# Kernel optimization log

Hardware: AMD Instinct MI355X
Metric: run time of the kernel (lower is better)

## Reference

```python
import jax, jax.numpy as jnp
import numpy as np

HEADS = 4
DIM_HEAD = 32
SCALE = 10.0
EPS = 1e-12

def l2norm_axis1(t):
    # Faithful to source: default axis=1 -> normalize over the SEQUENCE axis of [B,N,h,d]
    denom = jnp.clip(jnp.linalg.norm(t, ord=2, axis=1, keepdims=True), EPS)
    return t / denom

def setup_inputs() -> dict:
    key = jax.random.key(0)
    k1, k2, k3 = jax.random.split(key, 3)
    B, N, C = 4, 4096, 128
    dim = HEADS * DIM_HEAD  # 128
    x = jax.random.normal(k1, (B, N, C), dtype=jnp.float32)
    W_qkv = jax.random.normal(k2, (C, 3 * dim), dtype=jnp.float32) * (1.0 / np.sqrt(C))
    W_out = jax.random.normal(k3, (dim, C), dtype=jnp.float32) * (1.0 / np.sqrt(dim))
    b_out = jnp.zeros((C,), dtype=jnp.float32)
    return {"x": x, "W_qkv": W_qkv, "W_out": W_out, "b_out": b_out}

def reference(x, W_qkv, W_out, b_out):
    B, N, C = x.shape
    # 1x1 conv == per-token linear
    qkv = jnp.einsum('bnc,ce->bne', x, W_qkv)  # [B,N,3*dim]
    q, k, v = jnp.split(qkv, 3, axis=-1)
    # [B,N,h,d]
    q = q.reshape(B, N, HEADS, DIM_HEAD)
    k = k.reshape(B, N, HEADS, DIM_HEAD)
    v = v.reshape(B, N, HEADS, DIM_HEAD)
    q = l2norm_axis1(q)
    k = l2norm_axis1(k)
    sim = jnp.einsum('bihd,bjhd->bhij', q, k) * SCALE  # [B,h,N,N]
    attn = jax.nn.softmax(sim, axis=-1)
    out = jnp.einsum('bhij,bjhd->bhid', attn, v)  # [B,h,N,d]
    out = out.transpose(0, 2, 1, 3).reshape(B, N, HEADS * DIM_HEAD)  # [B,N,dim]
    return jnp.einsum('bne,ec->bnc', out, W_out) + b_out
```

## Files before the change

kernel.cpp:

```cpp
#include <hip/hip_runtime.h>

typedef short s16x8 __attribute__((ext_vector_type(8)));
typedef short s16x4 __attribute__((ext_vector_type(4)));
typedef float f32x4 __attribute__((ext_vector_type(4)));
typedef float f4 __attribute__((ext_vector_type(4)));
typedef unsigned short u16x4 __attribute__((ext_vector_type(4)));

#define CEXP 14.426950408889634074f

__device__ __forceinline__ unsigned short f2bf(float f) {
    union { float f; unsigned int i; } v; v.f = f;
    unsigned int x = v.i;
    return (unsigned short)((x + 0x7fffu + ((x >> 16) & 1u)) >> 16);
}
__device__ __forceinline__ float bf2f(unsigned short u) {
    union { unsigned int i; float f; } v; v.i = ((unsigned int)u) << 16; return v.f;
}

__device__ __forceinline__ f32x4 mfma16x16x16_bf16(s16x4 a, s16x4 b, f32x4 c) {
#if __has_builtin(__builtin_amdgcn_mfma_f32_16x16x16bf16_1k)
    return __builtin_amdgcn_mfma_f32_16x16x16bf16_1k(a, b, c, 0, 0, 0);
#else
    f32x4 d = c;
    asm("v_mfma_f32_16x16x16_bf16 %0, %1, %2, %0" : "+v"(d) : "v"(a), "v"(b));
    return d;
#endif
}

__global__ __launch_bounds__(256) void k_prep(
    const float* __restrict__ x, const float* __restrict__ Wqkv,
    const float* __restrict__ Wout,
    unsigned short* __restrict__ xb, unsigned short* __restrict__ Wt,
    unsigned short* __restrict__ WoT)
{
    const int blk = blockIdx.x, tid = threadIdx.x;
    if (blk < 1024) {
        int base = (blk * 256 + tid) * 8;
        f4 a = *(const f4*)&x[base];
        f4 b = *(const f4*)&x[base + 4];
        u16x4 p0 = { f2bf(a[0]), f2bf(a[1]), f2bf(a[2]), f2bf(a[3]) };
        u16x4 p1 = { f2bf(b[0]), f2bf(b[1]), f2bf(b[2]), f2bf(b[3]) };
        *(u16x4*)&xb[base] = p0;
        *(u16x4*)&xb[base + 4] = p1;
    } else if (blk < 1216) {
        int e = (blk - 1024) * 256 + tid;
        int n = e >> 7, k = e & 127;
        Wt[e] = f2bf(Wqkv[k * 384 + n]);
    } else {
        int e = (blk - 1216) * 256 + tid;
        int n = e >> 7, k = e & 127;
        WoT[e] = f2bf(Wout[k * 128 + n]);
    }
}

__global__ __launch_bounds__(256, 4) void k_qkv(
    const unsigned short* __restrict__ xb, const unsigned short* __restrict__ Wt,
    unsigned short* __restrict__ Qb, unsigned short* __restrict__ Kb,
    unsigned short* __restrict__ Vt, float* __restrict__ sumsq)
{
    const int tid = threadIdx.x;
    const int wl = tid >> 6, lane = tid & 63;
    const int qd = lane >> 4, nn = lane & 15;
    const int n0 = blockIdx.y * 64;
    const int tw0 = blockIdx.x * 64 + wl * 16;

    f32x4 acc[4];
#pragma unroll
    for (int nb = 0; nb < 4; ++nb) acc[nb] = (f32x4){0.f, 0.f, 0.f, 0.f};

    const unsigned short* ap = xb + (size_t)(tw0 + nn) * 128 + qd * 8;
    const unsigned short* bp = Wt + (size_t)(n0 + nn) * 128 + qd * 8;
#pragma unroll
    for (int ks = 0; ks < 4; ++ks) {
        s16x8 af = *(const s16x8*)(ap + ks * 32);
#pragma unroll
        for (int nb = 0; nb < 4; ++nb) {
            s16x8 bf = *(const s16x8*)(bp + (size_t)nb * 16 * 128 + ks * 32);
            acc[nb] = __builtin_amdgcn_mfma_f32_16x16x32_bf16(af, bf, acc[nb], 0, 0, 0);
        }
    }

    const int cb = n0 >> 7;
    const int cbase = n0 & 127;
    const int b = tw0 >> 12;
    const int tl0 = tw0 & 4095;

    if (cb < 2) {
        unsigned short* dst = (cb == 0) ? Qb : Kb;
#pragma unroll
        for (int nb = 0; nb < 4; ++nb) {
            const int dim = cbase + nb * 16 + nn;
            const int h = dim >> 5, d = dim & 31;
            unsigned short* base = dst + (size_t)((b * 4 + h) * 4096 + tl0 + qd * 4) * 32 + d;
#pragma unroll
            for (int r = 0; r < 4; ++r)
                base[r * 32] = f2bf(acc[nb][r]);
            float ss = acc[nb][0]*acc[nb][0] + acc[nb][1]*acc[nb][1]
                     + acc[nb][2]*acc[nb][2] + acc[nb][3]*acc[nb][3];
            ss += __shfl_xor(ss, 16);
            ss += __shfl_xor(ss, 32);
            if (qd == 0)
                atomicAdd(&sumsq[cb * 512 + (b * 4 + h) * 32 + d], ss);
        }
    } else {
#pragma unroll
        for (int nb = 0; nb < 4; ++nb) {
            const int dim = cbase + nb * 16 + nn;
            const int h = dim >> 5, d = dim & 31;
            u16x4 pk = { f2bf(acc[nb][0]), f2bf(acc[nb][1]),
                         f2bf(acc[nb][2]), f2bf(acc[nb][3]) };
            *(u16x4*)&Vt[(size_t)((b * 4 + h) * 32 + d) * 4096 + tl0 + qd * 4] = pk;
        }
    }
}

__global__ __launch_bounds__(256) void k_norm(
    unsigned short* __restrict__ Qb, unsigned short* __restrict__ Kb,
    const float* __restrict__ sumsq)
{
    int t = blockIdx.x * 256 + threadIdx.x;
    int which = t >> 18;
    int ti = t & 0x3ffff;
    unsigned short* arr = which ? Kb : Qb;
    const float post = which ? 1.0f : CEXP;
    int i8 = ti * 8;
    int d0 = i8 & 31;
    int bh = i8 >> 17;
    const float* sq = sumsq + which * 512 + bh * 32 + d0;
    union { uint4 v; unsigned short u[8]; } dat;
    dat.v = *(const uint4*)(arr + i8);
#pragma unroll
    for (int j = 0; j < 8; ++j) {
        float r = fminf(__builtin_amdgcn_rsqf(sq[j]), 1e12f) * post;
        dat.u[j] = f2bf(bf2f(dat.u[j]) * r);
    }
    *(uint4*)(arr + i8) = dat.v;
}

__global__ __launch_bounds__(512, 4) void k_attn(
    const unsigned short* __restrict__ Qb, const unsigned short* __restrict__ Kb,
    const unsigned short* __restrict__ Vt, unsigned short* __restrict__ Ogb)
{
    __shared__ char smem[32768];
    const int tid  = threadIdx.x;
    const int wv   = tid >> 6, lane = tid & 63;
    const int wl   = wv & 3, half = wv >> 2;
    const int qd   = lane >> 4, nn = lane & 15;
    const int bh   = blockIdx.x;
    const int ib   = blockIdx.y * 64 + wl * 16;
    const unsigned short* Qbh = Qb + (size_t)bh * 4096 * 32;
    const unsigned short* Kbh = Kb + (size_t)bh * 4096 * 32;
    const unsigned short* Vbh = Vt + (size_t)bh * 32 * 4096;

    s16x8 qfrag = *(const s16x8*)(Qbh + (ib + nn) * 32 + qd * 8);
    f32x4 o0 = {0.f,0.f,0.f,0.f}, o1 = {0.f,0.f,0.f,0.f};
    const f32x4 zro = {0.f,0.f,0.f,0.f};
    float lp = 0.f;

    const int KB0 = half * 8192;
    const int VB0 = 16384 + half * 8192;
    const int jb0 = half * 2048;

    const unsigned short* ksrc = Kbh + (size_t)(jb0 + wl * 16 + nn) * 32 + qd * 8;
    const unsigned short* vsrc = Vbh + (size_t)(nn + 16 * (wl >> 1)) * 4096
                               + jb0 + ((wl & 1) * 2 + (qd >> 1)) * 16 + (qd & 1) * 8;
    char* kdst = smem + KB0 + wl * 1024 + lane * 16;
    char* vdst = smem + VB0 + wl * 1024 + lane * 16;

    {
        uint4 gk = *(const uint4*)ksrc;
        uint4 gv = *(const uint4*)vsrc;
        ksrc += 2048; vsrc += 64;
        *(uint4*)kdst = gk;
        *(uint4*)vdst = gv;
    }

    const int vro = (qd >> 1) * 256 + nn * 16 + (qd & 1) * 8;

    for (int jt = 0; jt < 32; ++jt) {
        uint4 ngk = *(const uint4*)ksrc;
        uint4 ngv = *(const uint4*)vsrc;
        ksrc += 2048; vsrc += 64;

        __syncthreads();
        const char* kcur = smem + KB0 + (jt & 1) * 4096;
        const char* vcur = smem + VB0 + (jt & 1) * 4096;
#pragma unroll
        for (int js = 0; js < 4; ++js) {
            s16x8 kf = *(const s16x8*)(kcur + js * 1024 + lane * 16);
            f32x4 sv = __builtin_amdgcn_mfma_f32_16x16x32_bf16(kf, qfrag, zro, 0, 0, 0);
            float p0 = __builtin_amdgcn_exp2f(sv[0]);
            float p1 = __builtin_amdgcn_exp2f(sv[1]);
            float p2 = __builtin_amdgcn_exp2f(sv[2]);
            float p3 = __builtin_amdgcn_exp2f(sv[3]);
            lp += (p0 + p1) + (p2 + p3);
            unsigned u0 = __float_as_uint(p0) + 0x8000u;
            unsigned u1 = __float_as_uint(p1) + 0x8000u;
            unsigned u2 = __float_as_uint(p2) + 0x8000u;
            unsigned u3 = __float_as_uint(p3) + 0x8000u;
            union { uint2 u; s16x4 s; } pb;
            pb.u.x = __builtin_amdgcn_perm(u1, u0, 0x07060302u);
            pb.u.y = __builtin_amdgcn_perm(u3, u2, 0x07060302u);
            s16x4 va = *(const s16x4*)(vcur + js * 512 + vro);
            s16x4 vb = *(const s16x4*)(vcur + 2048 + js * 512 + vro);
            o0 = mfma16x16x16_bf16(va, pb.s, o0);
            o1 = mfma16x16x16_bf16(vb, pb.s, o1);
        }
        const int nxt4k = ((jt + 1) & 1) * 4096;
        *(uint4*)(kdst + nxt4k) = ngk;
        *(uint4*)(vdst + nxt4k) = ngv;
    }

    lp += __shfl_xor(lp, 16);
    lp += __shfl_xor(lp, 32);
    __syncthreads();
    float* Ob = (float*)smem;
    float* Lb = (float*)(smem + 8192);
    if (half) {
        float* d = Ob + (wl * 64 + lane) * 8;
        *(f4*)d = o0; *(f4*)(d + 4) = o1;
        Lb[wl * 64 + lane] = lp;
    }
    __syncthreads();
    if (!half) {
        float* d = Ob + (wl * 64 + lane) * 8;
        f4 a0 = *(const f4*)d, a1 = *(const f4*)(d + 4);
        float rl = 1.f / (lp + Lb[wl * 64 + lane]);
        o0 = (o0 + a0) * rl;
        o1 = (o1 + a1) * rl;
        u16x4 pk0 = { f2bf(o0[0]), f2bf(o0[1]), f2bf(o0[2]), f2bf(o0[3]) };
        u16x4 pk1 = { f2bf(o1[0]), f2bf(o1[1]), f2bf(o1[2]), f2bf(o1[3]) };
        const int bb = bh >> 2, hh = bh & 3;
        unsigned short* dst = Ogb + (size_t)(bb * 4096 + blockIdx.y * 64 + wl * 16 + nn) * 128
                            + hh * 32 + qd * 4;
        *(u16x4*)dst = pk0;
        *(u16x4*)(dst + 16) = pk1;
    }
}

__global__ __launch_bounds__(256, 4) void k_out(
    const unsigned short* __restrict__ Ogb, const unsigned short* __restrict__ WoT,
    const float* __restrict__ bout, float* __restrict__ out)
{
    const int tid = threadIdx.x;
    const int wl = tid >> 6, lane = tid & 63;
    const int qd = lane >> 4, nn = lane & 15;
    const int n0 = blockIdx.y * 64;
    const int tw0 = blockIdx.x * 64 + wl * 16;

    f32x4 acc[4];
#pragma unroll
    for (int nb = 0; nb < 4; ++nb) acc[nb] = (f32x4){0.f, 0.f, 0.f, 0.f};

    const unsigned short* ap = WoT + (size_t)(n0 + nn) * 128 + qd * 8;
    const unsigned short* bp = Ogb + (size_t)(tw0 + nn) * 128 + qd * 8;
#pragma unroll
    for (int ks = 0; ks < 4; ++ks) {
        s16x8 bf = *(const s16x8*)(bp + ks * 32);
#pragma unroll
        for (int nb = 0; nb < 4; ++nb) {
            s16x8 af = *(const s16x8*)(ap + (size_t)nb * 16 * 128 + ks * 32);
            acc[nb] = __builtin_amdgcn_mfma_f32_16x16x32_bf16(af, bf, acc[nb], 0, 0, 0);
        }
    }
#pragma unroll
    for (int nb = 0; nb < 4; ++nb) {
        const int c = n0 + nb * 16 + qd * 4;
        f4 bv = *(const f4*)&bout[c];
        f4 r;
#pragma unroll
        for (int j = 0; j < 4; ++j) r[j] = acc[nb][j] + bv[j];
        *(f4*)&out[(size_t)(tw0 + nn) * 128 + c] = r;
    }
}

extern "C" void kernel_launch(void* const* d_in, const int* in_sizes, int n_in,
                              void* d_out, int out_size, void* d_ws, size_t ws_size,
                              hipStream_t stream)
{
    const float* x    = (const float*)d_in[0];
    const float* Wqkv = (const float*)d_in[1];
    const float* Wout = (const float*)d_in[2];
    const float* bout = (const float*)d_in[3];
    float* out = (float*)d_out;
    char* ws = (char*)d_ws;
    const size_t MB = 1024 * 1024;
    unsigned short* Qb  = (unsigned short*)(ws);
    unsigned short* Kb  = (unsigned short*)(ws + 4 * MB);
    unsigned short* Vt  = (unsigned short*)(ws + 8 * MB);
    unsigned short* Ogb = (unsigned short*)(ws + 12 * MB);
    unsigned short* xb  = (unsigned short*)(ws + 16 * MB);
    unsigned short* Wt  = (unsigned short*)(ws + 20 * MB);
    unsigned short* WoT = (unsigned short*)(ws + 20 * MB + 112 * 1024);
    float*        sumsq = (float*)(ws + 20 * MB + 160 * 1024);

    hipMemsetAsync(sumsq, 0, 4096, stream);
    hipLaunchKernelGGL(k_prep, dim3(1280), dim3(256), 0, stream, x, Wqkv, Wout, xb, Wt, WoT);
    hipLaunchKernelGGL(k_qkv, dim3(256, 6), dim3(256), 0, stream, xb, Wt, Qb, Kb, Vt, sumsq);
    hipLaunchKernelGGL(k_norm, dim3(2048), dim3(256), 0, stream, Qb, Kb, sumsq);
    hipLaunchKernelGGL(k_attn, dim3(16, 64), dim3(512), 0, stream, Qb, Kb, Vt, Ogb);
    hipLaunchKernelGGL(k_out, dim3(256, 2), dim3(256), 0, stream, Ogb, WoT, bout, out);
}
```

Before: 169.1 us.

## Process two query tiles per wave in attention and fold Q normalization in

After: 189.8 us. 12.2% more time.

```diff
diff --git a/kernel.cpp b/kernel.cpp
--- a/kernel.cpp
+++ b/kernel.cpp
@@ -27,6 +27,30 @@
 #endif
 }
 
+__device__ __forceinline__ s16x4 pk_bf16x4(float p0, float p1, float p2, float p3) {
+#if __has_builtin(__builtin_amdgcn_cvt_pk_bf16_f32)
+    typedef __bf16 bf16x2 __attribute__((ext_vector_type(2)));
+    union { struct { bf16x2 a, b; } h; s16x4 s; } r;
+    r.h.a = __builtin_amdgcn_cvt_pk_bf16_f32(p0, p1);
+    r.h.b = __builtin_amdgcn_cvt_pk_bf16_f32(p2, p3);
+    return r.s;
+#else
+    unsigned u0 = __float_as_uint(p0) + 0x8000u;
+    unsigned u1 = __float_as_uint(p1) + 0x8000u;
+    unsigned u2 = __float_as_uint(p2) + 0x8000u;
+    unsigned u3 = __float_as_uint(p3) + 0x8000u;
+    union { uint2 u; s16x4 s; } pb;
+    pb.u.x = __builtin_amdgcn_perm(u1, u0, 0x07060302u);
+    pb.u.y = __builtin_amdgcn_perm(u3, u2, 0x07060302u);
+    return pb.s;
+#endif
+}
+
+__device__ __forceinline__ u16x4 pk4(f4 v) {
+    u16x4 r = { f2bf(v[0]), f2bf(v[1]), f2bf(v[2]), f2bf(v[3]) };
+    return r;
+}
+
 __global__ __launch_bounds__(256) void k_prep(
     const float* __restrict__ x, const float* __restrict__ Wqkv,
     const float* __restrict__ Wout,
@@ -38,10 +62,8 @@
         int base = (blk * 256 + tid) * 8;
         f4 a = *(const f4*)&x[base];
         f4 b = *(const f4*)&x[base + 4];
-        u16x4 p0 = { f2bf(a[0]), f2bf(a[1]), f2bf(a[2]), f2bf(a[3]) };
-        u16x4 p1 = { f2bf(b[0]), f2bf(b[1]), f2bf(b[2]), f2bf(b[3]) };
-        *(u16x4*)&xb[base] = p0;
-        *(u16x4*)&xb[base + 4] = p1;
+        *(u16x4*)&xb[base] = pk4(a);
+        *(u16x4*)&xb[base + 4] = pk4(b);
     } else if (blk < 1216) {
         int e = (blk - 1024) * 256 + tid;
         int n = e >> 7, k = e & 127;
@@ -64,82 +86,91 @@
     const int n0 = blockIdx.y * 64;
     const int tw0 = blockIdx.x * 64 + wl * 16;
 
-    f32x4 acc[4];
-#pragma unroll
-    for (int nb = 0; nb < 4; ++nb) acc[nb] = (f32x4){0.f, 0.f, 0.f, 0.f};
-
     const unsigned short* ap = xb + (size_t)(tw0 + nn) * 128 + qd * 8;
     const unsigned short* bp = Wt + (size_t)(n0 + nn) * 128 + qd * 8;
-#pragma unroll
-    for (int ks = 0; ks < 4; ++ks) {
-        s16x8 af = *(const s16x8*)(ap + ks * 32);
-#pragma unroll
-        for (int nb = 0; nb < 4; ++nb) {
-            s16x8 bf = *(const s16x8*)(bp + (size_t)nb * 16 * 128 + ks * 32);
-            acc[nb] = __builtin_amdgcn_mfma_f32_16x16x32_bf16(af, bf, acc[nb], 0, 0, 0);
-        }
-    }
+    s16x8 af[4], bfr[16];
+#pragma unroll
+    for (int ks = 0; ks < 4; ++ks) af[ks] = *(const s16x8*)(ap + ks * 32);
+#pragma unroll
+    for (int nb = 0; nb < 4; ++nb)
+#pragma unroll
+        for (int ks = 0; ks < 4; ++ks)
+            bfr[nb * 4 + ks] = *(const s16x8*)(bp + (size_t)nb * 2048 + ks * 32);
+
+    f32x4 acc[4];
+#pragma unroll
+    for (int nb = 0; nb < 4; ++nb) acc[nb] = (f32x4){0.f, 0.f, 0.f, 0.f};
 
     const int cb = n0 >> 7;
-    const int cbase = n0 & 127;
     const int b = tw0 >> 12;
     const int tl0 = tw0 & 4095;
 
     if (cb < 2) {
+#pragma unroll
+        for (int ks = 0; ks < 4; ++ks)
+#pragma unroll
+            for (int nb = 0; nb < 4; ++nb)
+                acc[nb] = __builtin_amdgcn_mfma_f32_16x16x32_bf16(bfr[nb * 4 + ks], af[ks], acc[nb], 0, 0, 0);
         unsigned short* dst = (cb == 0) ? Qb : Kb;
+        const int tok = tl0 + nn;
 #pragma unroll
         for (int nb = 0; nb < 4; ++nb) {
-            const int dim = cbase + nb * 16 + nn;
-            const int h = dim >> 5, d = dim & 31;
-            unsigned short* base = dst + (size_t)((b * 4 + h) * 4096 + tl0 + qd * 4) * 32 + d;
-#pragma unroll
-            for (int r = 0; r < 4; ++r)
-                base[r * 32] = f2bf(acc[nb][r]);
-            float ss = acc[nb][0]*acc[nb][0] + acc[nb][1]*acc[nb][1]
-                     + acc[nb][2]*acc[nb][2] + acc[nb][3]*acc[nb][3];
-            ss += __shfl_xor(ss, 16);
-            ss += __shfl_xor(ss, 32);
-            if (qd == 0)
-                atomicAdd(&sumsq[cb * 512 + (b * 4 + h) * 32 + d], ss);
+            const int dim = (n0 & 127) + nb * 16 + qd * 4;
+            const int h = dim >> 5, d0 = dim & 31;
+            *(u16x4*)&dst[(size_t)((b * 4 + h) * 4096 + tok) * 32 + d0] = pk4(acc[nb]);
+            f32x4 ss;
+#pragma unroll
+            for (int r = 0; r < 4; ++r) ss[r] = acc[nb][r] * acc[nb][r];
+#pragma unroll
+            for (int m = 1; m < 16; m <<= 1) {
+#pragma unroll
+                for (int r = 0; r < 4; ++r) ss[r] += __shfl_xor(ss[r], m);
+            }
+            if (nn == 0) {
+                float* sp = &sumsq[cb * 512 + (b * 4 + h) * 32 + d0];
+                atomicAdd(sp + 0, ss[0]);
+                atomicAdd(sp + 1, ss[1]);
+                atomicAdd(sp + 2, ss[2]);
+                atomicAdd(sp + 3, ss[3]);
+            }
         }
     } else {
 #pragma unroll
+        for (int ks = 0; ks < 4; ++ks)
+#pragma unroll
+            for (int nb = 0; nb < 4; ++nb)
+                acc[nb] = __builtin_amdgcn_mfma_f32_16x16x32_bf16(af[ks], bfr[nb * 4 + ks], acc[nb], 0, 0, 0);
+#pragma unroll
         for (int nb = 0; nb < 4; ++nb) {
-            const int dim = cbase + nb * 16 + nn;
+            const int dim = (n0 & 127) + nb * 16 + nn;
             const int h = dim >> 5, d = dim & 31;
-            u16x4 pk = { f2bf(acc[nb][0]), f2bf(acc[nb][1]),
-                         f2bf(acc[nb][2]), f2bf(acc[nb][3]) };
-            *(u16x4*)&Vt[(size_t)((b * 4 + h) * 32 + d) * 4096 + tl0 + qd * 4] = pk;
+            *(u16x4*)&Vt[(size_t)((b * 4 + h) * 32 + d) * 4096 + tl0 + qd * 4] = pk4(acc[nb]);
         }
     }
 }
 
 __global__ __launch_bounds__(256) void k_norm(
-    unsigned short* __restrict__ Qb, unsigned short* __restrict__ Kb,
-    const float* __restrict__ sumsq)
+    unsigned short* __restrict__ Kb, const float* __restrict__ sumsq)
 {
     int t = blockIdx.x * 256 + threadIdx.x;
-    int which = t >> 18;
-    int ti = t & 0x3ffff;
-    unsigned short* arr = which ? Kb : Qb;
-    const float post = which ? 1.0f : CEXP;
-    int i8 = ti * 8;
+    int i8 = t * 8;
     int d0 = i8 & 31;
     int bh = i8 >> 17;
-    const float* sq = sumsq + which * 512 + bh * 32 + d0;
+    const float* sq = sumsq + 512 + bh * 32 + d0;
     union { uint4 v; unsigned short u[8]; } dat;
-    dat.v = *(const uint4*)(arr + i8);
+    dat.v = *(const uint4*)(Kb + i8);
 #pragma unroll
     for (int j = 0; j < 8; ++j) {
-        float r = fminf(__builtin_amdgcn_rsqf(sq[j]), 1e12f) * post;
+        float r = fminf(__builtin_amdgcn_rsqf(sq[j]), 1e12f);
         dat.u[j] = f2bf(bf2f(dat.u[j]) * r);
     }
-    *(uint4*)(arr + i8) = dat.v;
-}
-
-__global__ __launch_bounds__(512, 4) void k_attn(
+    *(uint4*)(Kb + i8) = dat.v;
+}
+
+__global__ __launch_bounds__(512, 2) void k_attn(
     const unsigned short* __restrict__ Qb, const unsigned short* __restrict__ Kb,
-    const unsigned short* __restrict__ Vt, unsigned short* __restrict__ Ogb)
+    const unsigned short* __restrict__ Vt, const float* __restrict__ sumsq,
+    unsigned short* __restrict__ Ogb)
 {
     __shared__ char smem[32768];
     const int tid  = threadIdx.x;
@@ -147,15 +178,30 @@
     const int wl   = wv & 3, half = wv >> 2;
     const int qd   = lane >> 4, nn = lane & 15;
     const int bh   = blockIdx.x;
-    const int ib   = blockIdx.y * 64 + wl * 16;
+    const int ib   = blockIdx.y * 128 + wl * 32;
     const unsigned short* Qbh = Qb + (size_t)bh * 4096 * 32;
     const unsigned short* Kbh = Kb + (size_t)bh * 4096 * 32;
     const unsigned short* Vbh = Vt + (size_t)bh * 32 * 4096;
 
-    s16x8 qfrag = *(const s16x8*)(Qbh + (ib + nn) * 32 + qd * 8);
-    f32x4 o0 = {0.f,0.f,0.f,0.f}, o1 = {0.f,0.f,0.f,0.f};
+    float rj[8];
+    const float* sqq = sumsq + bh * 32 + qd * 8;
+#pragma unroll
+    for (int j = 0; j < 8; ++j)
+        rj[j] = fminf(__builtin_amdgcn_rsqf(sqq[j]), 1e12f) * CEXP;
+
+    s16x8 q0r = *(const s16x8*)(Qbh + (ib + nn) * 32 + qd * 8);
+    s16x8 q1r = *(const s16x8*)(Qbh + (ib + 16 + nn) * 32 + qd * 8);
+    s16x8 qf0, qf1;
+#pragma unroll
+    for (int j = 0; j < 8; ++j) {
+        qf0[j] = (short)f2bf(bf2f((unsigned short)q0r[j]) * rj[j]);
+        qf1[j] = (short)f2bf(bf2f((unsigned short)q1r[j]) * rj[j]);
+    }
+
+    f32x4 o00 = {0.f,0.f,0.f,0.f}, o01 = {0.f,0.f,0.f,0.f};
+    f32x4 o10 = {0.f,0.f,0.f,0.f}, o11 = {0.f,0.f,0.f,0.f};
     const f32x4 zro = {0.f,0.f,0.f,0.f};
-    float lp = 0.f;
+    float lpa = 0.f, lpb = 0.f;
 
     const int KB0 = half * 8192;
     const int VB0 = 16384 + half * 8192;
@@ -188,53 +234,65 @@
 #pragma unroll
         for (int js = 0; js < 4; ++js) {
             s16x8 kf = *(const s16x8*)(kcur + js * 1024 + lane * 16);
-            f32x4 sv = __builtin_amdgcn_mfma_f32_16x16x32_bf16(kf, qfrag, zro, 0, 0, 0);
-            float p0 = __builtin_amdgcn_exp2f(sv[0]);
-            float p1 = __builtin_amdgcn_exp2f(sv[1]);
-            float p2 = __builtin_amdgcn_exp2f(sv[2]);
-            float p3 = __builtin_amdgcn_exp2f(sv[3]);
-            lp += (p0 + p1) + (p2 + p3);
-            unsigned u0 = __float_as_uint(p0) + 0x8000u;
-            unsigned u1 = __float_as_uint(p1) + 0x8000u;
-            unsigned u2 = __float_as_uint(p2) + 0x8000u;
-            unsigned u3 = __float_as_uint(p3) + 0x8000u;
-            union { uint2 u; s16x4 s; } pb;
-            pb.u.x = __builtin_amdgcn_perm(u1, u0, 0x07060302u);
-            pb.u.y = __builtin_amdgcn_perm(u3, u2, 0x07060302u);
+            f32x4 sa = __builtin_amdgcn_mfma_f32_16x16x32_bf16(kf, qf0, zro, 0, 0, 0);
+            f32x4 sb = __builtin_amdgcn_mfma_f32_16x16x32_bf16(kf, qf1, zro, 0, 0, 0);
+            float a0 = __builtin_amdgcn_exp2f(sa[0]);
+            float a1 = __builtin_amdgcn_exp2f(sa[1]);
+            float a2 = __builtin_amdgcn_exp2f(sa[2]);
+            float a3 = __builtin_amdgcn_exp2f(sa[3]);
+            float b0 = __builtin_amdgcn_exp2f(sb[0]);
+            float b1 = __builtin_amdgcn_exp2f(sb[1]);
+            float b2 = __builtin_amdgcn_exp2f(sb[2]);
+            float b3 = __builtin_amdgcn_exp2f(sb[3]);
+            lpa += (a0 + a1) + (a2 + a3);
+            lpb += (b0 + b1) + (b2 + b3);
+            s16x4 pa = pk_bf16x4(a0, a1, a2, a3);
+            s16x4 pb = pk_bf16x4(b0, b1, b2, b3);
             s16x4 va = *(const s16x4*)(vcur + js * 512 + vro);
             s16x4 vb = *(const s16x4*)(vcur + 2048 + js * 512 + vro);
-            o0 = mfma16x16x16_bf16(va, pb.s, o0);
-            o1 = mfma16x16x16_bf16(vb, pb.s, o1);
+            o00 = mfma16x16x16_bf16(va, pa, o00);
+            o01 = mfma16x16x16_bf16(vb, pa, o01);
+            o10 = mfma16x16x16_bf16(va, pb, o10);
+            o11 = mfma16x16x16_bf16(vb, pb, o11);
         }
         const int nxt4k = ((jt + 1) & 1) * 4096;
         *(uint4*)(kdst + nxt4k) = ngk;
         *(uint4*)(vdst + nxt4k) = ngv;
     }
 
-    lp += __shfl_xor(lp, 16);
-    lp += __shfl_xor(lp, 32);
+    lpa += __shfl_xor(lpa, 16);
+    lpa += __shfl_xor(lpa, 32);
+    lpb += __shfl_xor(lpb, 16);
+    lpb += __shfl_xor(lpb, 32);
     __syncthreads();
     float* Ob = (float*)smem;
-    float* Lb = (float*)(smem + 8192);
+    float* Lb = (float*)(smem + 16384);
     if (half) {
-        float* d = Ob + (wl * 64 + lane) * 8;
-        *(f4*)d = o0; *(f4*)(d + 4) = o1;
-        Lb[wl * 64 + lane] = lp;
+        float* d0 = Ob + ((wl * 2 + 0) * 64 + lane) * 8;
+        *(f4*)d0 = o00; *(f4*)(d0 + 4) = o01;
+        float* d1 = Ob + ((wl * 2 + 1) * 64 + lane) * 8;
+        *(f4*)d1 = o10; *(f4*)(d1 + 4) = o11;
+        Lb[(wl * 2 + 0) * 64 + lane] = lpa;
+        Lb[(wl * 2 + 1) * 64 + lane] = lpb;
     }
     __syncthreads();
     if (!half) {
-        float* d = Ob + (wl * 64 + lane) * 8;
-        f4 a0 = *(const f4*)d, a1 = *(const f4*)(d + 4);
-        float rl = 1.f / (lp + Lb[wl * 64 + lane]);
-        o0 = (o0 + a0) * rl;
-        o1 = (o1 + a1) * rl;
-        u16x4 pk0 = { f2bf(o0[0]), f2bf(o0[1]), f2bf(o0[2]), f2bf(o0[3]) };
-        u16x4 pk1 = { f2bf(o1[0]), f2bf(o1[1]), f2bf(o1[2]), f2bf(o1[3]) };
         const int bb = bh >> 2, hh = bh & 3;
-        unsigned short* dst = Ogb + (size_t)(bb * 4096 + blockIdx.y * 64 + wl * 16 + nn) * 128
-                            + hh * 32 + qd * 4;
-        *(u16x4*)dst = pk0;
-        *(u16x4*)(dst + 16) = pk1;
+        float* s0 = Ob + ((wl * 2 + 0) * 64 + lane) * 8;
+        float rla = 1.f / (lpa + Lb[(wl * 2 + 0) * 64 + lane]);
+        f4 m00 = (o00 + *(const f4*)s0) * rla;
+        f4 m01 = (o01 + *(const f4*)(s0 + 4)) * rla;
+        float* s1 = Ob + ((wl * 2 + 1) * 64 + lane) * 8;
+        float rlb = 1.f / (lpb + Lb[(wl * 2 + 1) * 64 + lane]);
+        f4 m10 = (o10 + *(const f4*)s1) * rlb;
+        f4 m11 = (o11 + *(const f4*)(s1 + 4)) * rlb;
+        unsigned short* dst0 = Ogb + (size_t)(bb * 4096 + blockIdx.y * 128 + wl * 32 + nn) * 128
+                             + hh * 32 + qd * 4;
+        *(u16x4*)dst0 = pk4(m00);
+        *(u16x4*)(dst0 + 16) = pk4(m01);
+        unsigned short* dst1 = dst0 + (size_t)16 * 128;
+        *(u16x4*)dst1 = pk4(m10);
+        *(u16x4*)(dst1 + 16) = pk4(m11);
     }
 }
 
@@ -248,21 +306,26 @@
     const int n0 = blockIdx.y * 64;
     const int tw0 = blockIdx.x * 64 + wl * 16;
 
-    f32x4 acc[4];
-#pragma unroll
-    for (int nb = 0; nb < 4; ++nb) acc[nb] = (f32x4){0.f, 0.f, 0.f, 0.f};
-
     const unsigned short* ap = WoT + (size_t)(n0 + nn) * 128 + qd * 8;
     const unsigned short* bp = Ogb + (size_t)(tw0 + nn) * 128 + qd * 8;
-#pragma unroll
-    for (int ks = 0; ks < 4; ++ks) {
-        s16x8 bf = *(const s16x8*)(bp + ks * 32);
-#pragma unroll
-        for (int nb = 0; nb < 4; ++nb) {
-            s16x8 af = *(const s16x8*)(ap + (size_t)nb * 16 * 128 + ks * 32);
-            acc[nb] = __builtin_amdgcn_mfma_f32_16x16x32_bf16(af, bf, acc[nb], 0, 0, 0);
-        }
-    }
+    s16x8 bfr[4], afr[16];
+#pragma unroll
+    for (int ks = 0; ks < 4; ++ks) bfr[ks] = *(const s16x8*)(bp + ks * 32);
+#pragma unroll
+    for (int nb = 0; nb < 4; ++nb)
+#pragma unroll
+        for (int ks = 0; ks < 4; ++ks)
+            afr[nb * 4 + ks] = *(const s16x8*)(ap + (size_t)nb * 2048 + ks * 32);
+
+    f32x4 acc[4];
+#pragma unroll
+    for (int nb = 0; nb < 4; ++nb) acc[nb] = (f32x4){0.f, 0.f, 0.f, 0.f};
+#pragma unroll
+    for (int ks = 0; ks < 4; ++ks)
+#pragma unroll
+        for (int nb = 0; nb < 4; ++nb)
+            acc[nb] = __builtin_amdgcn_mfma_f32_16x16x32_bf16(afr[nb * 4 + ks], bfr[ks], acc[nb], 0, 0, 0);
+
 #pragma unroll
     for (int nb = 0; nb < 4; ++nb) {
         const int c = n0 + nb * 16 + qd * 4;
@@ -297,7 +360,7 @@
     hipMemsetAsync(sumsq, 0, 4096, stream);
     hipLaunchKernelGGL(k_prep, dim3(1280), dim3(256), 0, stream, x, Wqkv, Wout, xb, Wt, WoT);
     hipLaunchKernelGGL(k_qkv, dim3(256, 6), dim3(256), 0, stream, xb, Wt, Qb, Kb, Vt, sumsq);
-    hipLaunchKernelGGL(k_norm, dim3(2048), dim3(256), 0, stream, Qb, Kb, sumsq);
-    hipLaunchKernelGGL(k_attn, dim3(16, 64), dim3(512), 0, stream, Qb, Kb, Vt, Ogb);
+    hipLaunchKernelGGL(k_norm, dim3(1024), dim3(256), 0, stream, Kb, sumsq);
+    hipLaunchKernelGGL(k_attn, dim3(16, 32), dim3(512), 0, stream, Qb, Kb, Vt, sumsq, Ogb);
     hipLaunchKernelGGL(k_out, dim3(256, 2), dim3(256), 0, stream, Ogb, WoT, bout, out);
 }
```
